# Optimization experiments

Measured on AMD Instinct MI355X. Metric: run time of the kernel, lower is better.

## Reference

```python
import jax, jax.numpy as jnp
import numpy as np
import math

B, T, C = 4, 1024, 1024
H = 16          # n_head
E = 8           # num_experts
K = 2           # top_k
HID = 4096      # expert_hidden_dim
TEMP = 1.0
EPS_LN = 1e-5


def setup_inputs() -> dict:
    key = jax.random.key(0)
    ks = jax.random.split(key, 16)
    s = 0.02
    return {
        'x': jax.random.normal(ks[0], (B, T, C), jnp.float32),
        'ln1_g': jnp.ones((C,), jnp.float32),
        'ln1_b': jnp.zeros((C,), jnp.float32),
        'W_qkv': jax.random.normal(ks[1], (C, 3 * C), jnp.float32) * s,
        'b_qkv': jnp.zeros((3 * C,), jnp.float32),
        'W_proj': jax.random.normal(ks[2], (C, C), jnp.float32) * s,
        'b_proj': jnp.zeros((C,), jnp.float32),
        'ln2_g': jnp.ones((C,), jnp.float32),
        'ln2_b': jnp.zeros((C,), jnp.float32),
        'W_router': jax.random.normal(ks[3], (C, E), jnp.float32) * s,
        'W1': jax.random.normal(ks[4], (E, C, HID), jnp.float32) * s,
        'b1': jnp.zeros((E, HID), jnp.float32),
        'W2': jax.random.normal(ks[5], (E, HID, C), jnp.float32) * s,
        'b2': jnp.zeros((E, C), jnp.float32),
    }


def _layernorm(x, g, b):
    mu = jnp.mean(x, axis=-1, keepdims=True)
    var = jnp.mean(jnp.square(x - mu), axis=-1, keepdims=True)
    return (x - mu) * jax.lax.rsqrt(var + EPS_LN) * g + b


def reference(x, ln1_g, ln1_b, W_qkv, b_qkv, W_proj, b_proj,
              ln2_g, ln2_b, W_router, W1, b1, W2, b2):
    D = C // H
    # --- causal self-attention on ln_1(x) ---
    h = _layernorm(x, ln1_g, ln1_b)
    qkv = h @ W_qkv + b_qkv                      # [B,T,3C]
    q, k, v = jnp.split(qkv, 3, axis=-1)
    q = q.reshape(B, T, H, D).transpose(0, 2, 1, 3)   # [B,H,T,D]
    k = k.reshape(B, T, H, D).transpose(0, 2, 1, 3)
    v = v.reshape(B, T, H, D).transpose(0, 2, 1, 3)
    att = jnp.einsum('bhqd,bhkd->bhqk', q, k) * (1.0 / math.sqrt(D))
    mask = jnp.tril(jnp.ones((T, T), bool))
    att = jnp.where(mask, att, -jnp.inf)
    att = jax.nn.softmax(att, axis=-1)
    y = jnp.einsum('bhqk,bhkd->bhqd', att, v)
    y = y.transpose(0, 2, 1, 3).reshape(B, T, C)
    x = x + (y @ W_proj + b_proj)

    # --- sparse MoE on ln_2(x) ---
    h2 = _layernorm(x, ln2_g, ln2_b)
    xf = h2.reshape(-1, C)                       # [N,C]
    N = xf.shape[0]
    logits = (xf @ W_router) / TEMP              # [N,E]
    prob = jax.nn.softmax(logits, axis=-1)
    top_prob, top_idx = jax.lax.top_k(prob, K)   # [N,K]
    top_prob = top_prob / (jnp.sum(top_prob, axis=-1, keepdims=True) + 1e-9)
    # dense per-token per-expert combine weights (0 for unselected experts)
    w = jnp.zeros((N, E), xf.dtype).at[jnp.arange(N)[:, None], top_idx].add(top_prob)
    # dense expert compute (weights zero out unselected experts -> same math)
    hid = jax.nn.gelu(jnp.einsum('nc,ech->neh', xf, W1) + b1, approximate=False)
    eo = jnp.einsum('neh,ehc->nec', hid, W2) + b2          # [N,E,C]
    out_flat = jnp.einsum('nec,ne->nc', eo, w)
    x = x + out_flat.reshape(B, T, C)

    counts = jnp.zeros((E,), jnp.float32).at[top_idx.reshape(-1)].add(1.0)
    expert_utilization = counts / (jnp.sum(counts) + 1e-9)
    return x, expert_utilization
```

## Files before the change

### kernel.cpp

```cpp
#include <hip/hip_runtime.h>
#include <cmath>

#define CDIM 1024
#define NTOK 4096
#define NHEAD 16
#define HDIM 64
#define NEXP 8
#define HIDD 4096
#define MAXROWS 9216

typedef short bf16x8 __attribute__((ext_vector_type(8)));
typedef short s16x4  __attribute__((ext_vector_type(4)));
typedef float f32x4  __attribute__((ext_vector_type(4)));

static __device__ __forceinline__ short f2bf(float f){
  unsigned u = __builtin_bit_cast(unsigned, f);
  u += 0x7fffu + ((u >> 16) & 1u);
  return (short)(u >> 16);
}

static __device__ __forceinline__ int swz64(int r, int ch){
  return r*64 + (((ch ^ (r>>1)) & 3) << 4);
}
static __device__ __forceinline__ int swz128(int r, int ch){
  return r*128 + (((ch ^ r) & 7) << 4);
}

static __device__ __forceinline__ void gl16(const short* g, short* l){
  __builtin_amdgcn_global_load_lds(
      (const __attribute__((address_space(1))) void*)g,
      (__attribute__((address_space(3))) void*)l, 16, 0, 0);
}

__global__ void k_transpose_cast(const float* __restrict__ in, short* __restrict__ out,
                                 int R, int Cc){
  __shared__ float tile[64][65];
  const int z = blockIdx.z;
  const float* src = in + (long long)z*R*Cc;
  short* dst = out + (long long)z*R*Cc;
  const int r0 = blockIdx.y*64, c0 = blockIdx.x*64;
  const int t = threadIdx.x;
  #pragma unroll
  for (int it=0; it<4; ++it){
    const int item = t + it*256;
    const int r = item>>4, c4 = item&15;
    const float4 v = *(const float4*)(src + (long long)(r0+r)*Cc + c0 + c4*4);
    tile[r][c4*4+0]=v.x; tile[r][c4*4+1]=v.y; tile[r][c4*4+2]=v.z; tile[r][c4*4+3]=v.w;
  }
  __syncthreads();
  #pragma unroll
  for (int it=0; it<2; ++it){
    const int item = t + it*256;
    const int rr8 = item & 7, cc = item >> 3;
    bf16x8 o;
    #pragma unroll
    for (int i=0;i<8;i++) o[i] = f2bf(tile[rr8*8+i][cc]);
    *(bf16x8*)(dst + (long long)(c0+cc)*R + r0 + rr8*8) = o;
  }
}

__global__ void k_ln1(const float* __restrict__ x, const float* __restrict__ g,
                      const float* __restrict__ b, short* __restrict__ out){
  const int row = blockIdx.x;
  const int t = threadIdx.x;
  const float4 v = ((const float4*)(x + (long long)row*CDIM))[t];
  float s  = v.x+v.y+v.z+v.w;
  float s2 = v.x*v.x+v.y*v.y+v.z*v.z+v.w*v.w;
  #pragma unroll
  for (int mm=1; mm<64; mm<<=1){ s += __shfl_xor(s,mm); s2 += __shfl_xor(s2,mm); }
  __shared__ float ps[4], ps2[4];
  const int w = t>>6, l = t&63;
  if (l==0){ ps[w]=s; ps2[w]=s2; }
  __syncthreads();
  s  = ps[0]+ps[1]+ps[2]+ps[3];
  s2 = ps2[0]+ps2[1]+ps2[2]+ps2[3];
  const float mu = s*(1.f/CDIM);
  const float rstd = rsqrtf(s2*(1.f/CDIM) - mu*mu + 1e-5f);
  const float4 gg = ((const float4*)g)[t];
  const float4 bb = ((const float4*)b)[t];
  s16x4 o;
  o[0]=f2bf((v.x-mu)*rstd*gg.x+bb.x); o[1]=f2bf((v.y-mu)*rstd*gg.y+bb.y);
  o[2]=f2bf((v.z-mu)*rstd*gg.z+bb.z); o[3]=f2bf((v.w-mu)*rstd*gg.w+bb.w);
  *(s16x4*)(out + (long long)row*CDIM + t*4) = o;
}

__global__ void k_ln2_router(const float* __restrict__ x1, const float* __restrict__ g,
                             const float* __restrict__ b, const float* __restrict__ Wr,
                             short* __restrict__ h2, int* __restrict__ tidx,
                             float* __restrict__ tw, int* __restrict__ counts){
  const int row = blockIdx.x;
  const int t = threadIdx.x;
  const float4 v = ((const float4*)(x1 + (long long)row*CDIM))[t];
  float s  = v.x+v.y+v.z+v.w;
  float s2 = v.x*v.x+v.y*v.y+v.z*v.z+v.w*v.w;
  #pragma unroll
  for (int mm=1; mm<64; mm<<=1){ s += __shfl_xor(s,mm); s2 += __shfl_xor(s2,mm); }
  __shared__ float ps[4], ps2[4];
  const int w = t>>6, l = t&63;
  if (l==0){ ps[w]=s; ps2[w]=s2; }
  __syncthreads();
  s  = ps[0]+ps[1]+ps[2]+ps[3];
  s2 = ps2[0]+ps2[1]+ps2[2]+ps2[3];
  const float mu = s*(1.f/CDIM);
  const float rstd = rsqrtf(s2*(1.f/CDIM) - mu*mu + 1e-5f);
  const float4 gg = ((const float4*)g)[t];
  const float4 bb = ((const float4*)b)[t];
  const float y0=(v.x-mu)*rstd*gg.x+bb.x, y1=(v.y-mu)*rstd*gg.y+bb.y;
  const float y2=(v.z-mu)*rstd*gg.z+bb.z, y3=(v.w-mu)*rstd*gg.w+bb.w;
  s16x4 o; o[0]=f2bf(y0); o[1]=f2bf(y1); o[2]=f2bf(y2); o[3]=f2bf(y3);
  *(s16x4*)(h2 + (long long)row*CDIM + t*4) = o;

  float acc[8];
  const float* wr0 = Wr + (long long)(t*4)*NEXP;
  #pragma unroll
  for (int e=0;e<8;e++) acc[e] = y0*wr0[e] + y1*wr0[8+e] + y2*wr0[16+e] + y3*wr0[24+e];
  #pragma unroll
  for (int mm=1; mm<64; mm<<=1){
    #pragma unroll
    for (int e=0;e<8;e++) acc[e] += __shfl_xor(acc[e], mm);
  }
  __shared__ float pl[4][8];
  if (l==0){
    #pragma unroll
    for (int e=0;e<8;e++) pl[w][e]=acc[e];
  }
  __syncthreads();
  if (t==0){
    float lg[8];
    #pragma unroll
    for (int e=0;e<8;e++) lg[e] = pl[0][e]+pl[1][e]+pl[2][e]+pl[3][e];
    float mx = lg[0];
    #pragma unroll
    for (int e=1;e<8;e++) mx = fmaxf(mx, lg[e]);
    float pr[8]; float sum = 0.f;
    #pragma unroll
    for (int e=0;e<8;e++){ pr[e]=expf(lg[e]-mx); sum += pr[e]; }
    int i0 = 0;
    #pragma unroll
    for (int e=1;e<8;e++) if (pr[e] > pr[i0]) i0 = e;
    int i1 = (i0==0) ? 1 : 0;
    #pragma unroll
    for (int e=0;e<8;e++) if (e!=i0 && pr[e] > pr[i1]) i1 = e;
    const float p0 = pr[i0]/sum, p1 = pr[i1]/sum;
    const float dn = p0 + p1 + 1e-9f;
    tidx[row*2]=i0; tidx[row*2+1]=i1;
    tw[row*2]=p0/dn; tw[row*2+1]=p1/dn;
    atomicAdd(&counts[i0],1); atomicAdd(&counts[i1],1);
  }
}

__global__ void k_route_setup(const int* __restrict__ counts, int* __restrict__ offs,
                              int* __restrict__ cursors, int* __restrict__ rowmap,
                              float* __restrict__ util){
  if (threadIdx.x == 0){
    int o = 0;
    for (int e=0;e<8;e++){
      offs[e] = o; cursors[e] = o;
      o += (counts[e] + 127) & ~127;
    }
    offs[8] = o;
    for (int e=0;e<8;e++) util[e] = (float)counts[e] / 8192.0f;
  }
  for (int i = threadIdx.x; i < MAXROWS; i += blockDim.x) rowmap[i] = -1;
}

__global__ void k_scatter(const int* __restrict__ tidx, const float* __restrict__ tw,
                          int* __restrict__ cursors, int* __restrict__ rowmap,
                          float* __restrict__ roww, int* __restrict__ posmap){
  const int i = blockIdx.x*blockDim.x + threadIdx.x;
  if (i >= 2*NTOK) return;
  const int e = tidx[i];
  const int pos = atomicAdd(&cursors[e], 1);
  rowmap[pos] = i >> 1;
  roww[pos]   = tw[i];
  posmap[i]   = pos;
}

template<int EPI>
__launch_bounds__(256)
__global__ void k_gemm(const short* __restrict__ A, const short* __restrict__ Bt,
                       const float* __restrict__ bias, const float* __restrict__ resid,
                       void* __restrict__ Cout, int N, int K,
                       const int* __restrict__ rowmap, const int* __restrict__ offs,
                       long long expStrideB, const short* __restrict__ zrow){
  int wg = blockIdx.x;
  const int nwg = gridDim.x;
  {
    const int q = nwg >> 3, r8 = nwg & 7;
    const int xcd = wg & 7, pos = wg >> 3;
    wg = (xcd < r8 ? xcd*(q+1) : r8*(q+1) + (xcd - r8)*q) + pos;
  }
  const int gridN = N >> 7;
  const int gridM = nwg / gridN;
  const int mtile = wg % gridM, ntile = wg / gridM;
  const int mbase = mtile*128;
  const int nbase = ntile*128;
  int e = 0;
  if constexpr (EPI >= 2){
    if (mbase >= offs[8]) return;
    while (e < 7 && mbase >= offs[e+1]) e++;
    Bt += (long long)e * expStrideB;
  }
  __shared__ short Asm[128*32];
  __shared__ short Bsm[128*32];
  const int tid = threadIdx.x;
  const int w = tid >> 6, l = tid & 63;
  const int wr = w >> 1, wc = w & 1;
  const int l15 = l & 15, l4 = l >> 4;

  const short* aSrc[2]; const short* bSrc[2];
  short* aDst[2]; short* bDst[2];
  #pragma unroll
  for (int inst=0; inst<2; ++inst){
    const int g = w*128 + inst*64 + l;
    const int r = g >> 2, ch = g & 3;
    const int sch = (ch ^ (r >> 1)) & 3;
    if constexpr (EPI == 2){
      const int grow = rowmap[mbase + r];
      aSrc[inst] = (grow >= 0) ? (A + (long long)grow*K + sch*8) : (zrow + sch*8);
    } else {
      aSrc[inst] = A + (long long)(mbase + r)*K + sch*8;
    }
    bSrc[inst] = Bt + (long long)(nbase + r)*K + sch*8;
    aDst[inst] = Asm + w*1024 + inst*512;
    bDst[inst] = Bsm + w*1024 + inst*512;
  }

  f32x4 acc[4][4];
  const f32x4 z4 = {0.f,0.f,0.f,0.f};
  #pragma unroll
  for (int i=0;i<4;i++){
    #pragma unroll
    for (int jn=0;jn<4;jn++) acc[i][jn] = z4;
  }

  for (int kt = 0; kt < K; kt += 32){
    #pragma unroll
    for (int inst=0; inst<2; ++inst){
      gl16(aSrc[inst] + kt, aDst[inst]);
      gl16(bSrc[inst] + kt, bDst[inst]);
    }
    __syncthreads();
    bf16x8 af[4], bfr[4];
    #pragma unroll
    for (int i=0;i<4;i++){
      af[i]  = *(const bf16x8*)((char*)Asm + swz64(wr*64 + i*16 + l15, l4));
      bfr[i] = *(const bf16x8*)((char*)Bsm + swz64(wc*64 + i*16 + l15, l4));
    }
    #pragma unroll
    for (int i=0;i<4;i++){
      #pragma unroll
      for (int jn=0;jn<4;jn++)
        acc[i][jn] = __builtin_amdgcn_mfma_f32_16x16x32_bf16(af[i], bfr[jn], acc[i][jn], 0,0,0);
    }
    __syncthreads();
  }

  #pragma unroll
  for (int i=0;i<4;i++){
    const int row0 = mbase + wr*64 + i*16 + l4*4;
    #pragma unroll
    for (int jn=0;jn<4;jn++){
      const int col = nbase + wc*64 + jn*16 + l15;
      const float bi = bias[(EPI>=2 ? e*N : 0) + col];
      #pragma unroll
      for (int j=0;j<4;j++){
        const long long idx = (long long)(row0 + j)*N + col;
        float v = acc[i][jn][j] + bi;
        if constexpr (EPI == 0){
          ((short*)Cout)[idx] = f2bf(v);
        } else if constexpr (EPI == 1){
          ((float*)Cout)[idx] = v + resid[idx];
        } else if constexpr (EPI == 2){
          ((short*)Cout)[idx] = f2bf(0.5f*v*(1.0f + erff(v*0.70710678118654752f)));
        } else {
          ((float*)Cout)[idx] = v;
        }
      }
    }
  }
}

__launch_bounds__(256)
__global__ void k_attn(const short* __restrict__ qkv, short* __restrict__ y){
  const int qt = blockIdx.x;
  const int bh = blockIdx.y;
  const int bb = bh >> 4;
  const int h  = bh & 15;
  const int tid = threadIdx.x;
  const int w = tid >> 6, l = tid & 63;
  const int l15 = l & 15, l4 = l >> 4;

  __shared__ short Ksm[64*64];
  __shared__ short Vtsm[64*64];
  __shared__ short Psm[4*16*64];

  const long long rs = 3*CDIM;
  const int qrow0 = bb*1024 + qt*64;

  bf16x8 aq[2];
  {
    const int qr = qrow0 + w*16 + l15;
    const short* qp = qkv + (long long)qr*rs + h*HDIM;
    aq[0] = *(const bf16x8*)(qp + l4*8);
    aq[1] = *(const bf16x8*)(qp + 32 + l4*8);
  }

  const f32x4 z4 = {0.f,0.f,0.f,0.f};
  f32x4 O[4];
  #pragma unroll
  for (int cf=0;cf<4;cf++) O[cf] = z4;
  float mrow[4], lrow[4];
  #pragma unroll
  for (int j=0;j<4;j++){ mrow[j] = -1e30f; lrow[j] = 0.f; }

  for (int kvb = 0; kvb <= qt; ++kvb){
    const int kvrow0 = bb*1024 + kvb*64;
    #pragma unroll
    for (int p=0;p<2;p++){
      const int ch = tid + p*256;
      const int r = ch >> 3, c = ch & 7;
      const short* kp = qkv + (long long)(kvrow0 + r)*rs + CDIM + h*HDIM + c*8;
      *(bf16x8*)((char*)Ksm + swz128(r, c)) = *(const bf16x8*)kp;
      const short* vp = qkv + (long long)(kvrow0 + r)*rs + 2*CDIM + h*HDIM + c*8;
      bf16x8 vv = *(const bf16x8*)vp;
      const int off2 = 2*r;
      const int g0 = off2 >> 4, b0 = off2 & 15;
      #pragma unroll
      for (int i=0;i<8;i++){
        const int d = c*8 + i;
        *(short*)((char*)Vtsm + d*128 + (((g0 ^ d) & 7) << 4) + b0) = vv[i];
      }
    }
    __syncthreads();

    f32x4 S[4];
    #pragma unroll
    for (int cf=0;cf<4;cf++) S[cf] = z4;
    #pragma unroll
    for (int cf=0;cf<4;cf++){
      #pragma unroll
      for (int kf=0;kf<2;kf++){
        bf16x8 bk = *(const bf16x8*)((char*)Ksm + swz128(cf*16 + l15, kf*4 + l4));
        S[cf] = __builtin_amdgcn_mfma_f32_16x16x32_bf16(aq[kf], bk, S[cf], 0,0,0);
      }
    }

    const bool diag = (kvb == qt);
    #pragma unroll
    for (int cf=0;cf<4;cf++){
      #pragma unroll
      for (int j=0;j<4;j++){
        float s = S[cf][j] * 0.125f;
        if (diag && (cf*16 + l15 > w*16 + l4*4 + j)) s = -1e30f;
        S[cf][j] = s;
      }
    }

    float alpha[4];
    #pragma unroll
    for (int j=0;j<4;j++){
      float mx = fmaxf(fmaxf(S[0][j],S[1][j]), fmaxf(S[2][j],S[3][j]));
      #pragma unroll
      for (int mm=1; mm<16; mm<<=1) mx = fmaxf(mx, __shfl_xor(mx, mm));
      const float mnew = fmaxf(mrow[j], mx);
      const float al = expf(mrow[j] - mnew);
      float psum = 0.f;
      #pragma unroll
      for (int cf=0;cf<4;cf++){ float pp = expf(S[cf][j]-mnew); S[cf][j]=pp; psum += pp; }
      #pragma unroll
      for (int mm=1; mm<16; mm<<=1) psum += __shfl_xor(psum, mm);
      lrow[j] = lrow[j]*al + psum;
      mrow[j] = mnew; alpha[j] = al;
    }
    #pragma unroll
    for (int cf=0;cf<4;cf++){
      #pragma unroll
      for (int j=0;j<4;j++) O[cf][j] *= alpha[j];
    }

    char* pw = (char*)Psm + w*2048;
    #pragma unroll
    for (int cf=0;cf<4;cf++){
      #pragma unroll
      for (int j=0;j<4;j++){
        const int r = l4*4 + j;
        const int cb = (cf*16 + l15)*2;
        *(short*)(pw + r*128 + ((((cb>>4) ^ r) & 7)<<4) + (cb & 15)) = f2bf(S[cf][j]);
      }
    }
    bf16x8 pa[2];
    pa[0] = *(const bf16x8*)(pw + swz128(l15, l4));
    pa[1] = *(const bf16x8*)(pw + swz128(l15, 4 + l4));
    #pragma unroll
    for (int cf=0;cf<4;cf++){
      #pragma unroll
      for (int kf=0;kf<2;kf++){
        bf16x8 bv = *(const bf16x8*)((char*)Vtsm + swz128(cf*16 + l15, kf*4 + l4));
        O[cf] = __builtin_amdgcn_mfma_f32_16x16x32_bf16(pa[kf], bv, O[cf], 0,0,0);
      }
    }
    __syncthreads();
  }

  const int yr0 = qrow0 + w*16;
  #pragma unroll
  for (int cf=0;cf<4;cf++){
    #pragma unroll
    for (int j=0;j<4;j++){
      const int r = l4*4 + j;
      y[(long long)(yr0 + r)*CDIM + h*HDIM + cf*16 + l15] = f2bf(O[cf][j] / lrow[j]);
    }
  }
}

__global__ void k_combine(const float* __restrict__ x1, const float* __restrict__ eo,
                          const int* __restrict__ posmap, const float* __restrict__ roww,
                          float* __restrict__ out){
  const int row = blockIdx.x;
  const int t = threadIdx.x;
  const int p0 = posmap[row*2], p1 = posmap[row*2+1];
  const float w0 = roww[p0], w1 = roww[p1];
  const float4 a  = ((const float4*)(x1 + (long long)row*CDIM))[t];
  const float4 e0 = ((const float4*)(eo + (long long)p0*CDIM))[t];
  const float4 e1 = ((const float4*)(eo + (long long)p1*CDIM))[t];
  float4 r;
  r.x = a.x + w0*e0.x + w1*e1.x;
  r.y = a.y + w0*e0.y + w1*e1.y;
  r.z = a.z + w0*e0.z + w1*e1.z;
  r.w = a.w + w0*e0.w + w1*e1.w;
  ((float4*)(out + (long long)row*CDIM))[t] = r;
}

extern "C" void kernel_launch(void* const* d_in, const int* in_sizes, int n_in,
                              void* d_out, int out_size, void* d_ws, size_t ws_size,
                              hipStream_t stream){
  const float* x     = (const float*)d_in[0];
  const float* ln1_g = (const float*)d_in[1];
  const float* ln1_b = (const float*)d_in[2];
  const float* W_qkv = (const float*)d_in[3];
  const float* b_qkv = (const float*)d_in[4];
  const float* W_proj= (const float*)d_in[5];
  const float* b_proj= (const float*)d_in[6];
  const float* ln2_g = (const float*)d_in[7];
  const float* ln2_b = (const float*)d_in[8];
  const float* W_r   = (const float*)d_in[9];
  const float* W1    = (const float*)d_in[10];
  const float* b1    = (const float*)d_in[11];
  const float* W2    = (const float*)d_in[12];
  const float* b2    = (const float*)d_in[13];
  float* out = (float*)d_out;
  float* util = out + (long long)NTOK*CDIM;

  char* p = (char*)d_ws;
  auto alloc = [&](size_t bytes)->char*{
    char* r = p; p += (bytes + 255) & ~(size_t)255; return r;
  };
  short* Wt1   = (short*)alloc((size_t)NEXP*HIDD*CDIM*2);
  short* Wt2   = (short*)alloc((size_t)NEXP*CDIM*HIDD*2);
  float* x1    = (float*)alloc((size_t)NTOK*CDIM*4);
  short* h2    = (short*)alloc((size_t)NTOK*CDIM*2);
  short* hid   = (short*)alloc((size_t)MAXROWS*HIDD*2);
  int*   tidx  = (int*)alloc(2*NTOK*4);
  float* tw    = (float*)alloc(2*NTOK*4);
  int*   counts= (int*)alloc(256);
  int*   offs  = (int*)alloc(256);
  int*   curs  = (int*)alloc(256);
  int*   rowmap= (int*)alloc(MAXROWS*4);
  float* roww  = (float*)alloc(MAXROWS*4);
  int*   posmap= (int*)alloc(2*NTOK*4);
  short* zrow  = (short*)alloc(8192);
  char* transStart = p;
  short* WtQ = (short*)alloc((size_t)3*CDIM*CDIM*2);
  short* WtP = (short*)alloc((size_t)CDIM*CDIM*2);
  short* h   = (short*)alloc((size_t)NTOK*CDIM*2);
  short* qkv = (short*)alloc((size_t)NTOK*3*CDIM*2);
  short* y   = (short*)alloc((size_t)NTOK*CDIM*2);
  float* eo  = (float*)transStart;

  (void)hipMemsetAsync(counts, 0, 32, stream);
  (void)hipMemsetAsync(zrow, 0, 8192, stream);

  k_transpose_cast<<<dim3(3*CDIM/64, CDIM/64, 1), 256, 0, stream>>>(W_qkv, WtQ, CDIM, 3*CDIM);
  k_transpose_cast<<<dim3(CDIM/64, CDIM/64, 1),   256, 0, stream>>>(W_proj, WtP, CDIM, CDIM);
  k_transpose_cast<<<dim3(HIDD/64, CDIM/64, NEXP),256, 0, stream>>>(W1, Wt1, CDIM, HIDD);
  k_transpose_cast<<<dim3(CDIM/64, HIDD/64, NEXP),256, 0, stream>>>(W2, Wt2, HIDD, CDIM);

  k_ln1<<<NTOK, 256, 0, stream>>>(x, ln1_g, ln1_b, h);

  k_gemm<0><<<dim3((NTOK/128)*(3*CDIM/128)), 256, 0, stream>>>(
      h, WtQ, b_qkv, nullptr, qkv, 3*CDIM, CDIM, nullptr, nullptr, 0, nullptr);

  k_attn<<<dim3(1024/64, 4*NHEAD), 256, 0, stream>>>(qkv, y);

  k_gemm<1><<<dim3((NTOK/128)*(CDIM/128)), 256, 0, stream>>>(
      y, WtP, b_proj, x, x1, CDIM, CDIM, nullptr, nullptr, 0, nullptr);

  k_ln2_router<<<NTOK, 256, 0, stream>>>(x1, ln2_g, ln2_b, W_r, h2, tidx, tw, counts);
  k_route_setup<<<1, 256, 0, stream>>>(counts, offs, curs, rowmap, util);
  k_scatter<<<(2*NTOK)/256, 256, 0, stream>>>(tidx, tw, curs, rowmap, roww, posmap);

  k_gemm<2><<<dim3((MAXROWS/128)*(HIDD/128)), 256, 0, stream>>>(
      h2, Wt1, b1, nullptr, hid, HIDD, CDIM, rowmap, offs, (long long)HIDD*CDIM, zrow);
  k_gemm<3><<<dim3((MAXROWS/128)*(CDIM/128)), 256, 0, stream>>>(
      hid, Wt2, b2, nullptr, eo, CDIM, HIDD, nullptr, offs, (long long)CDIM*HIDD, zrow);

  k_combine<<<NTOK, 256, 0, stream>>>(x1, eo, posmap, roww, out);
}
```

Baseline: 698.0 us.

## Double-buffer LDS tiles in GEMM to overlap global loads with MFMA

Splits the GEMM shared-memory A/B tiles into two buffers. The next K-slice is prefetched via direct-to-LDS loads while MFMAs run on the current buffer, which removes one of the two barriers per iteration. It also raises wave priority around the MFMA block. This doubles LDS use per block, which may lower occupancy, and correctness now depends on the manual vmcnt waits plus barrier ordering.

```diff
diff --git a/kernel.cpp b/kernel.cpp
--- a/kernel.cpp
+++ b/kernel.cpp
@@ -201,15 +201,15 @@
     while (e < 7 && mbase >= offs[e+1]) e++;
     Bt += (long long)e * expStrideB;
   }
-  __shared__ short Asm[128*32];
-  __shared__ short Bsm[128*32];
+  __shared__ short Asm[2][4096];
+  __shared__ short Bsm[2][4096];
   const int tid = threadIdx.x;
   const int w = tid >> 6, l = tid & 63;
   const int wr = w >> 1, wc = w & 1;
   const int l15 = l & 15, l4 = l >> 4;
 
   const short* aSrc[2]; const short* bSrc[2];
-  short* aDst[2]; short* bDst[2];
+  int dOff[2];
   #pragma unroll
   for (int inst=0; inst<2; ++inst){
     const int g = w*128 + inst*64 + l;
@@ -222,8 +222,7 @@
       aSrc[inst] = A + (long long)(mbase + r)*K + sch*8;
     }
     bSrc[inst] = Bt + (long long)(nbase + r)*K + sch*8;
-    aDst[inst] = Asm + w*1024 + inst*512;
-    bDst[inst] = Bsm + w*1024 + inst*512;
+    dOff[inst] = w*1024 + inst*512;
   }
 
   f32x4 acc[4][4];
@@ -234,27 +233,43 @@
     for (int jn=0;jn<4;jn++) acc[i][jn] = z4;
   }
 
-  for (int kt = 0; kt < K; kt += 32){
+  auto stage = [&](int buf, int kt){
     #pragma unroll
     for (int inst=0; inst<2; ++inst){
-      gl16(aSrc[inst] + kt, aDst[inst]);
-      gl16(bSrc[inst] + kt, bDst[inst]);
-    }
-    __syncthreads();
+      gl16(aSrc[inst] + kt, &Asm[buf][dOff[inst]]);
+      gl16(bSrc[inst] + kt, &Bsm[buf][dOff[inst]]);
+    }
+  };
+  auto compute = [&](int buf){
     bf16x8 af[4], bfr[4];
     #pragma unroll
     for (int i=0;i<4;i++){
-      af[i]  = *(const bf16x8*)((char*)Asm + swz64(wr*64 + i*16 + l15, l4));
-      bfr[i] = *(const bf16x8*)((char*)Bsm + swz64(wc*64 + i*16 + l15, l4));
-    }
+      af[i]  = *(const bf16x8*)((char*)Asm[buf] + swz64(wr*64 + i*16 + l15, l4));
+      bfr[i] = *(const bf16x8*)((char*)Bsm[buf] + swz64(wc*64 + i*16 + l15, l4));
+    }
+    __builtin_amdgcn_s_setprio(1);
     #pragma unroll
     for (int i=0;i<4;i++){
       #pragma unroll
       for (int jn=0;jn<4;jn++)
         acc[i][jn] = __builtin_amdgcn_mfma_f32_16x16x32_bf16(af[i], bfr[jn], acc[i][jn], 0,0,0);
     }
-    __syncthreads();
-  }
+    __builtin_amdgcn_s_setprio(0);
+  };
+
+  stage(0, 0);
+  asm volatile("s_waitcnt vmcnt(0)" ::: "memory");
+  __builtin_amdgcn_s_barrier();
+
+  int cur = 0;
+  for (int kt = 32; kt < K; kt += 32){
+    stage(cur ^ 1, kt);
+    compute(cur);
+    asm volatile("s_waitcnt vmcnt(0)" ::: "memory");
+    __builtin_amdgcn_s_barrier();
+    cur ^= 1;
+  }
+  compute(cur);
 
   #pragma unroll
   for (int i=0;i<4;i++){
```

Result: no change. 686.1 us (-1.7%).
